# Optimization experiments

Measured on AMD Instinct MI355X. Metric: run time of the kernel, lower is better.

Reference implementation:

```python
import jax, jax.numpy as jnp
import numpy as np

H = 1024       # hidden_size
I = 1024       # intermediate_size
E = 16         # num_experts
K = 4          # experts_per_token
LIMIT = 7.0    # swiglu_limit
ALPHA = 1.702  # swiglu alpha
EPS = 1e-5     # rmsnorm eps


def setup_inputs() -> dict:
    key = jax.random.key(0)
    ks = jax.random.split(key, 8)
    x = jax.random.normal(ks[0], (2, 512, H), dtype=jnp.float32)
    norm_scale = jnp.ones((H,), dtype=jnp.float32)
    wg = jax.random.normal(ks[1], (H, E), dtype=jnp.float32) * 0.02
    bg = jax.random.normal(ks[2], (E,), dtype=jnp.float32) * 0.02
    w1 = jax.random.normal(ks[3], (E, H, 2 * I), dtype=jnp.float32) * 0.02
    b1 = jax.random.normal(ks[4], (E, 2 * I), dtype=jnp.float32) * 0.02
    w2 = jax.random.normal(ks[5], (E, I, H), dtype=jnp.float32) * 0.02
    b2 = jax.random.normal(ks[6], (E, H), dtype=jnp.float32) * 0.02
    return {"x": x, "norm_scale": norm_scale, "wg": wg, "bg": bg,
            "w1": w1, "b1": b1, "w2": w2, "b2": b2}


def reference(x, norm_scale, wg, bg, w1, b1, w2, b2):
    shape = x.shape
    xf = x.reshape(-1, shape[-1])                                   # [T, H]
    # RMSNorm (float32 math)
    xn = xf * jax.lax.rsqrt(jnp.mean(xf * xf, axis=-1, keepdims=True) + EPS) * norm_scale
    # router logits + top-k with softmax over selected logits
    logits = xn @ wg + bg                                           # [T, E]
    vals, idx = jax.lax.top_k(logits, K)                            # [T, K]
    gates = jax.nn.softmax(vals, axis=-1)                           # [T, K]
    # dense [T, E] gate matrix (exactly equivalent to gather/scatter grouped GEMM)
    gate_full = jnp.einsum('tke,tk->te', jax.nn.one_hot(idx, E, dtype=gates.dtype), gates)
    # expert FFN 1 + fused swiglu (interleaved gate/linear pairs)
    h = jnp.einsum('th,ehd->etd', xn, w1) + b1[:, None, :]          # [E, T, 2I]
    a = jnp.minimum(h[..., ::2], LIMIT)                             # gate branch
    b = jnp.clip(h[..., 1::2], -LIMIT, LIMIT)                       # linear branch
    s = a * jax.nn.sigmoid(ALPHA * a) * (b + 1.0)                   # [E, T, I]
    # expert FFN 2; gamma (gate) scales the full epilogue incl. bias
    y = jnp.einsum('eti,eih->eth', s, w2) + b2[:, None, :]          # [E, T, H]
    t = jnp.einsum('eth,te->th', y, gate_full)                      # scatter-combine
    return x + t.reshape(shape)
```

## Files before the change

### kernel.cpp

```cpp
#include <hip/hip_runtime.h>

#define NH 1024
#define NI2 2048
#define NI 1024
#define NE 16
#define NT 1024

static constexpr float LIMITF = 7.0f;
static constexpr float ALPHAF = 1.702f;
static constexpr float EPSF = 1e-5f;

typedef short bf16x8 __attribute__((ext_vector_type(8)));
typedef float f32x16 __attribute__((ext_vector_type(16)));

__device__ __forceinline__ unsigned short f2bf(float f) {
  unsigned int u = __builtin_bit_cast(unsigned int, f);
  u = (u + 0x7FFFu + ((u >> 16) & 1u)) >> 16;
  return (unsigned short)u;
}

typedef __attribute__((address_space(1))) const unsigned int as1_uint;
typedef __attribute__((address_space(3))) unsigned int as3_uint;
__device__ __forceinline__ void gload16(const void* g, void* l) {
  __builtin_amdgcn_global_load_lds((as1_uint*)g, (as3_uint*)l, 16, 0, 0);
}

__global__ __launch_bounds__(256) void k_init(const float* __restrict__ x,
                                              float* __restrict__ out) {
  int i = blockIdx.x * 256 + threadIdx.x;
  reinterpret_cast<float4*>(out)[i] = reinterpret_cast<const float4*>(x)[i];
}

__global__ __launch_bounds__(256) void k_norm_router(
    const float* __restrict__ x, const float* __restrict__ nsc,
    const float* __restrict__ wg, const float* __restrict__ bg,
    unsigned short* __restrict__ xn, int* __restrict__ topk_idx,
    float* __restrict__ topk_gate, int* __restrict__ counts) {
  int t = blockIdx.x;
  int tid = threadIdx.x;
  int wave = tid >> 6, lane = tid & 63;

  float4 v = reinterpret_cast<const float4*>(x + (size_t)t * NH)[tid];
  float ss = v.x * v.x + v.y * v.y + v.z * v.z + v.w * v.w;
  for (int off = 32; off; off >>= 1) ss += __shfl_xor(ss, off);

  __shared__ float red[4];
  __shared__ float redl[4][16];
  __shared__ float logits_s[16];
  if (lane == 0) red[wave] = ss;
  __syncthreads();
  float tot = red[0] + red[1] + red[2] + red[3];
  float r = rsqrtf(tot * (1.0f / NH) + EPSF);

  float4 sc = reinterpret_cast<const float4*>(nsc)[tid];
  float xv[4];
  xv[0] = v.x * r * sc.x;
  xv[1] = v.y * r * sc.y;
  xv[2] = v.z * r * sc.z;
  xv[3] = v.w * r * sc.w;

  ushort4 o;
  o.x = f2bf(xv[0]); o.y = f2bf(xv[1]); o.z = f2bf(xv[2]); o.w = f2bf(xv[3]);
  reinterpret_cast<ushort4*>(xn + (size_t)t * NH)[tid] = o;

  float acc[16];
#pragma unroll
  for (int e = 0; e < 16; e++) acc[e] = 0.f;
  int hbase = tid * 4;
#pragma unroll
  for (int i = 0; i < 4; i++) {
    const float4* wr = reinterpret_cast<const float4*>(wg + (size_t)(hbase + i) * NE);
#pragma unroll
    for (int j = 0; j < 4; j++) {
      float4 w = wr[j];
      acc[j * 4 + 0] += xv[i] * w.x;
      acc[j * 4 + 1] += xv[i] * w.y;
      acc[j * 4 + 2] += xv[i] * w.z;
      acc[j * 4 + 3] += xv[i] * w.w;
    }
  }
#pragma unroll
  for (int e = 0; e < 16; e++)
    for (int off = 32; off; off >>= 1) acc[e] += __shfl_xor(acc[e], off);
  if (lane == 0) {
#pragma unroll
    for (int e = 0; e < 16; e++) redl[wave][e] = acc[e];
  }
  __syncthreads();
  if (tid < 16)
    logits_s[tid] = redl[0][tid] + redl[1][tid] + redl[2][tid] + redl[3][tid] + bg[tid];
  __syncthreads();

  if (tid == 0) {
    float vals[16];
#pragma unroll
    for (int e = 0; e < 16; e++) vals[e] = logits_s[e];
    int sel[4]; float sv[4];
    unsigned used = 0;
    for (int k = 0; k < 4; k++) {
      float best = -1e30f; int bi = 0;
      for (int e = 0; e < 16; e++) {
        if (!((used >> e) & 1u) && vals[e] > best) { best = vals[e]; bi = e; }
      }
      used |= 1u << bi; sel[k] = bi; sv[k] = best;
    }
    float g[4], ssum = 0.f;
    for (int k = 0; k < 4; k++) { g[k] = __expf(sv[k] - sv[0]); ssum += g[k]; }
    for (int k = 0; k < 4; k++) {
      topk_idx[t * 4 + k] = sel[k];
      topk_gate[t * 4 + k] = g[k] / ssum;
      atomicAdd(&counts[sel[k]], 1);
    }
  }
}

__global__ void k_scan(const int* __restrict__ counts, int* __restrict__ offsets,
                       int* __restrict__ cursor) {
  if (blockIdx.x == 0 && threadIdx.x == 0) {
    int o = 0;
    for (int e = 0; e < NE; e++) {
      offsets[e] = o; cursor[e] = o;
      o += (counts[e] + 31) & ~31;
    }
  }
}

__global__ __launch_bounds__(256) void k_fill(const int* __restrict__ topk_idx,
                                              const float* __restrict__ topk_gate,
                                              int* __restrict__ cursor,
                                              int* __restrict__ rows_tok,
                                              float* __restrict__ rows_gate) {
  int idx = blockIdx.x * 256 + threadIdx.x;
  if (idx >= NT * 4) return;
  int e = topk_idx[idx];
  int slot = atomicAdd(&cursor[e], 1);
  rows_tok[slot] = idx >> 2;
  rows_gate[slot] = topk_gate[idx];
}

__global__ __launch_bounds__(256) void k_gather(
    const unsigned short* __restrict__ xn, const int* __restrict__ counts,
    const int* __restrict__ offsets, const int* __restrict__ rows_tok,
    unsigned short* __restrict__ xg) {
  int e = blockIdx.y;
  int g = blockIdx.x;
  int cnt = counts[e];
  if (g * 32 >= cnt) return;
  int tid = threadIdx.x;
  int r = tid & 31, kq = tid >> 5;
  int rowbase = offsets[e];
  int tok = rows_tok[rowbase + min(g * 32 + r, cnt - 1)];
  const uint4* src = reinterpret_cast<const uint4*>(xn + (size_t)tok * NH);
  uint4* dst = reinterpret_cast<uint4*>(
      xg + ((size_t)(rowbase >> 5) + g) * (128 * 32 * 8));
#pragma unroll
  for (int i = 0; i < 16; i++) {
    int ko = i * 8 + kq;
    dst[ko * 32 + r] = src[ko];
  }
}

template <int ROWSTRIDE>
__device__ __forceinline__ void stage_panel_async(
    const float* __restrict__ wsrc, unsigned short* __restrict__ panel,
    float* __restrict__ fbuf, int tid) {
  int colq = tid & 7;
  int rquot = tid >> 3;
  int col = tid & 31;
  int oct = tid >> 5;
  for (int r = 0; r < 8; r++) {
#pragma unroll
    for (int i = 0; i < 4; i++) {
      int row = r * 128 + i * 32 + rquot;
      gload16(wsrc + (size_t)row * ROWSTRIDE + colq * 4,
              (char*)fbuf + tid * 16 + i * 4096);
    }
    __syncthreads();
#pragma unroll
    for (int oo = 0; oo < 2; oo++) {
      int o = oct + oo * 8;
      float f[8];
#pragma unroll
      for (int j = 0; j < 8; j++) f[j] = fbuf[(o * 8 + j) * 32 + col];
      unsigned pk[4];
#pragma unroll
      for (int j = 0; j < 4; j++)
        pk[j] = (unsigned)f2bf(f[2 * j]) | ((unsigned)f2bf(f[2 * j + 1]) << 16);
      *reinterpret_cast<uint4*>(&panel[(size_t)((r * 16 + o) * 32 + col) * 8]) =
          *reinterpret_cast<const uint4*>(pk);
    }
    __syncthreads();
  }
}

__global__ __launch_bounds__(256) void k_ffn1(
    const unsigned short* __restrict__ xg, const float* __restrict__ w1,
    const float* __restrict__ b1, const int* __restrict__ counts,
    const int* __restrict__ offsets, unsigned short* __restrict__ s_tiled) {
  int b = blockIdx.x;
  int j = b >> 3;
  int e = (b & 7) + ((j >> 6) << 3);
  int n0 = (j & 63) * 32;
  int cnt = counts[e];
  if (cnt == 0) return;
  int rowbase = offsets[e];
  int tid = threadIdx.x;

  __shared__ __align__(16) unsigned short lds_b[128 * 32 * 8];
  __shared__ __align__(16) float lds_f[128 * 32];

  stage_panel_async<NI2>(w1 + (size_t)e * (NH * NI2) + n0, lds_b, lds_f, tid);

  int lane = tid & 63;
  int wave = tid >> 6;
  int lrow = lane & 31;
  int khalf = lane >> 5;

  float bias = b1[(size_t)e * NI2 + n0 + lrow];
  int parity = lrow & 1;

  for (int m0 = 0; m0 < cnt; m0 += 256) {
    int tb0 = m0 + wave * 32;
    int tb1 = m0 + 128 + wave * 32;
    const unsigned short* a0p =
        xg + ((size_t)((rowbase + tb0) >> 5) * 128 + khalf) * 256 + lrow * 8;

    f32x16 acc0 = {0.f,0.f,0.f,0.f,0.f,0.f,0.f,0.f,0.f,0.f,0.f,0.f,0.f,0.f,0.f,0.f};
    f32x16 acc1 = {0.f,0.f,0.f,0.f,0.f,0.f,0.f,0.f,0.f,0.f,0.f,0.f,0.f,0.f,0.f,0.f};
    bool dual = (m0 + 128) < cnt;

    if (dual) {
      const unsigned short* a1p =
          xg + ((size_t)((rowbase + tb1) >> 5) * 128 + khalf) * 256 + lrow * 8;
#pragma unroll 4
      for (int k2 = 0; k2 < 64; k2++) {
        bf16x8 av0 = *reinterpret_cast<const bf16x8*>(a0p + k2 * 512);
        bf16x8 av1 = *reinterpret_cast<const bf16x8*>(a1p + k2 * 512);
        bf16x8 bv = *reinterpret_cast<const bf16x8*>(
            &lds_b[(size_t)((k2 * 2 + khalf) * 32 + lrow) * 8]);
        acc0 = __builtin_amdgcn_mfma_f32_32x32x16_bf16(av0, bv, acc0, 0, 0, 0);
        acc1 = __builtin_amdgcn_mfma_f32_32x32x16_bf16(av1, bv, acc1, 0, 0, 0);
      }
    } else {
#pragma unroll 4
      for (int k2 = 0; k2 < 64; k2++) {
        bf16x8 av0 = *reinterpret_cast<const bf16x8*>(a0p + k2 * 512);
        bf16x8 bv = *reinterpret_cast<const bf16x8*>(
            &lds_b[(size_t)((k2 * 2 + khalf) * 32 + lrow) * 8]);
        acc0 = __builtin_amdgcn_mfma_f32_32x32x16_bf16(av0, bv, acc0, 0, 0, 0);
      }
    }

#pragma unroll
    for (int t2 = 0; t2 < 2; t2++) {
      if (t2 == 1 && !dual) break;
      f32x16 acc = t2 ? acc1 : acc0;
      int tb = t2 ? tb1 : tb0;
#pragma unroll
      for (int reg = 0; reg < 16; reg++) {
        float v = acc[reg] + bias;
        float p = __shfl_xor(v, 1);
        int row = (reg & 3) + 8 * (reg >> 2) + 4 * khalf;
        int m = tb + row;
        if (!parity && m < cnt) {
          float aa = fminf(v, LIMITF);
          float bb = fminf(fmaxf(p, -LIMITF), LIMITF);
          float sig = 1.0f / (1.0f + __expf(-ALPHAF * aa));
          float sval = aa * sig * (bb + 1.0f);
          int c = (n0 + lrow) >> 1;
          size_t grp = (size_t)(rowbase + tb) >> 5;
          s_tiled[(grp * 128 + (c >> 3)) * 256 + row * 8 + (c & 7)] = f2bf(sval);
        }
      }
    }
  }
}

__global__ __launch_bounds__(256) void k_ffn2(
    const unsigned short* __restrict__ s_tiled, const float* __restrict__ w2,
    const float* __restrict__ b2, const int* __restrict__ counts,
    const int* __restrict__ offsets, const int* __restrict__ rows_tok,
    const float* __restrict__ rows_gate, float* __restrict__ out) {
  int b = blockIdx.x;
  int j = b >> 3;
  int e = (b & 7) + ((j >> 5) << 3);
  int n0 = (j & 31) * 32;
  int cnt = counts[e];
  if (cnt == 0) return;
  int rowbase = offsets[e];
  int tid = threadIdx.x;

  __shared__ __align__(16) unsigned short lds_b[128 * 32 * 8];
  __shared__ __align__(16) float lds_f[128 * 32];

  stage_panel_async<NH>(w2 + (size_t)e * (NI * NH) + n0, lds_b, lds_f, tid);

  int lane = tid & 63;
  int wave = tid >> 6;
  int lrow = lane & 31;
  int khalf = lane >> 5;

  float b2v = b2[(size_t)e * NH + n0 + lrow];

  for (int m0 = 0; m0 < cnt; m0 += 256) {
    int tb0 = m0 + wave * 32;
    int tb1 = m0 + 128 + wave * 32;
    const unsigned short* a0p =
        s_tiled + ((size_t)((rowbase + tb0) >> 5) * 128 + khalf) * 256 + lrow * 8;

    f32x16 acc0 = {0.f,0.f,0.f,0.f,0.f,0.f,0.f,0.f,0.f,0.f,0.f,0.f,0.f,0.f,0.f,0.f};
    f32x16 acc1 = {0.f,0.f,0.f,0.f,0.f,0.f,0.f,0.f,0.f,0.f,0.f,0.f,0.f,0.f,0.f,0.f};
    bool dual = (m0 + 128) < cnt;

    if (dual) {
      const unsigned short* a1p =
          s_tiled + ((size_t)((rowbase + tb1) >> 5) * 128 + khalf) * 256 + lrow * 8;
#pragma unroll 4
      for (int k2 = 0; k2 < 64; k2++) {
        bf16x8 av0 = *reinterpret_cast<const bf16x8*>(a0p + k2 * 512);
        bf16x8 av1 = *reinterpret_cast<const bf16x8*>(a1p + k2 * 512);
        bf16x8 bv = *reinterpret_cast<const bf16x8*>(
            &lds_b[(size_t)((k2 * 2 + khalf) * 32 + lrow) * 8]);
        acc0 = __builtin_amdgcn_mfma_f32_32x32x16_bf16(av0, bv, acc0, 0, 0, 0);
        acc1 = __builtin_amdgcn_mfma_f32_32x32x16_bf16(av1, bv, acc1, 0, 0, 0);
      }
    } else {
#pragma unroll 4
      for (int k2 = 0; k2 < 64; k2++) {
        bf16x8 av0 = *reinterpret_cast<const bf16x8*>(a0p + k2 * 512);
        bf16x8 bv = *reinterpret_cast<const bf16x8*>(
            &lds_b[(size_t)((k2 * 2 + khalf) * 32 + lrow) * 8]);
        acc0 = __builtin_amdgcn_mfma_f32_32x32x16_bf16(av0, bv, acc0, 0, 0, 0);
      }
    }

#pragma unroll
    for (int t2 = 0; t2 < 2; t2++) {
      if (t2 == 1 && !dual) break;
      f32x16 acc = t2 ? acc1 : acc0;
      int tb = t2 ? tb1 : tb0;
#pragma unroll
      for (int reg = 0; reg < 16; reg++) {
        int row = (reg & 3) + 8 * (reg >> 2) + 4 * khalf;
        int m = tb + row;
        if (m < cnt) {
          int rr = rowbase + m;
          int tok = rows_tok[rr];
          float g = rows_gate[rr];
          atomicAdd(&out[(size_t)tok * NH + n0 + lrow], g * (acc[reg] + b2v));
        }
      }
    }
  }
}

extern "C" void kernel_launch(void* const* d_in, const int* in_sizes, int n_in,
                              void* d_out, int out_size, void* d_ws, size_t ws_size,
                              hipStream_t stream) {
  const float* x   = (const float*)d_in[0];
  const float* nsc = (const float*)d_in[1];
  const float* wg  = (const float*)d_in[2];
  const float* bg  = (const float*)d_in[3];
  const float* w1  = (const float*)d_in[4];
  const float* b1  = (const float*)d_in[5];
  const float* w2  = (const float*)d_in[6];
  const float* b2  = (const float*)d_in[7];
  float* out = (float*)d_out;
  char* ws = (char*)d_ws;

  int*   counts    = (int*)(ws + 0);
  int*   offsets   = (int*)(ws + 64);
  int*   cursor    = (int*)(ws + 128);
  int*   topk_idx  = (int*)(ws + 1024);
  float* topk_gate = (float*)(ws + 17408);
  int*   rows_tok  = (int*)(ws + 33792);
  float* rows_gate = (float*)(ws + 54272);
  unsigned short* xn      = (unsigned short*)(ws + 131072);
  unsigned short* xg      = (unsigned short*)(ws + 2228224);
  unsigned short* s_tiled = (unsigned short*)(ws + 12 * 1024 * 1024);

  hipMemsetAsync(ws, 0, 256, stream);
  k_init<<<NT * NH / 1024, 256, 0, stream>>>(x, out);
  k_norm_router<<<NT, 256, 0, stream>>>(x, nsc, wg, bg, xn, topk_idx, topk_gate,
                                        counts);
  k_scan<<<1, 64, 0, stream>>>(counts, offsets, cursor);
  k_fill<<<16, 256, 0, stream>>>(topk_idx, topk_gate, cursor, rows_tok, rows_gate);
  k_gather<<<dim3(128, NE), 256, 0, stream>>>(xn, counts, offsets, rows_tok, xg);
  k_ffn1<<<1024, 256, 0, stream>>>(xg, w1, b1, counts, offsets, s_tiled);
  k_ffn2<<<512, 256, 0, stream>>>(s_tiled, w2, b2, counts, offsets,
                                  rows_tok, rows_gate, out);
}
```

Measured before the change: 430.0 us.

## Use 512-thread blocks with one M-tile per wave and register-prefetched A operands

Both expert GEMM kernels now launch 8 waves per block instead of 4. Each wave handles a single 32-row tile rather than two, and the weight-panel staging is spread across 512 threads. The A-operand loads from global memory go through an 8-deep register prefetch ring, so MFMAs overlap with in-flight loads, aiming to hide global-load latency and raise occupancy. Risks: `__launch_bounds__(512,4)` may squeeze registers and cause spills, the prefetch reads past the end of the K range, and the LDS footprint may cap real occupancy anyway.

```diff
diff --git a/kernel.cpp b/kernel.cpp
--- a/kernel.cpp
+++ b/kernel.cpp
@@ -167,33 +167,29 @@
   int colq = tid & 7;
   int rquot = tid >> 3;
   int col = tid & 31;
-  int oct = tid >> 5;
+  int o = tid >> 5;
   for (int r = 0; r < 8; r++) {
 #pragma unroll
-    for (int i = 0; i < 4; i++) {
-      int row = r * 128 + i * 32 + rquot;
+    for (int i = 0; i < 2; i++) {
+      int row = r * 128 + i * 64 + rquot;
       gload16(wsrc + (size_t)row * ROWSTRIDE + colq * 4,
-              (char*)fbuf + tid * 16 + i * 4096);
+              (char*)fbuf + tid * 16 + i * 8192);
     }
     __syncthreads();
-#pragma unroll
-    for (int oo = 0; oo < 2; oo++) {
-      int o = oct + oo * 8;
-      float f[8];
-#pragma unroll
-      for (int j = 0; j < 8; j++) f[j] = fbuf[(o * 8 + j) * 32 + col];
-      unsigned pk[4];
-#pragma unroll
-      for (int j = 0; j < 4; j++)
-        pk[j] = (unsigned)f2bf(f[2 * j]) | ((unsigned)f2bf(f[2 * j + 1]) << 16);
-      *reinterpret_cast<uint4*>(&panel[(size_t)((r * 16 + o) * 32 + col) * 8]) =
-          *reinterpret_cast<const uint4*>(pk);
-    }
+    float f[8];
+#pragma unroll
+    for (int jj = 0; jj < 8; jj++) f[jj] = fbuf[(o * 8 + jj) * 32 + col];
+    unsigned pk[4];
+#pragma unroll
+    for (int jj = 0; jj < 4; jj++)
+      pk[jj] = (unsigned)f2bf(f[2 * jj]) | ((unsigned)f2bf(f[2 * jj + 1]) << 16);
+    *reinterpret_cast<uint4*>(&panel[(size_t)((r * 16 + o) * 32 + col) * 8]) =
+        *reinterpret_cast<const uint4*>(pk);
     __syncthreads();
   }
 }
 
-__global__ __launch_bounds__(256) void k_ffn1(
+__global__ __launch_bounds__(512, 4) void k_ffn1(
     const unsigned short* __restrict__ xg, const float* __restrict__ w1,
     const float* __restrict__ b1, const int* __restrict__ counts,
     const int* __restrict__ offsets, unsigned short* __restrict__ s_tiled) {
@@ -220,63 +216,47 @@
   int parity = lrow & 1;
 
   for (int m0 = 0; m0 < cnt; m0 += 256) {
-    int tb0 = m0 + wave * 32;
-    int tb1 = m0 + 128 + wave * 32;
-    const unsigned short* a0p =
-        xg + ((size_t)((rowbase + tb0) >> 5) * 128 + khalf) * 256 + lrow * 8;
-
-    f32x16 acc0 = {0.f,0.f,0.f,0.f,0.f,0.f,0.f,0.f,0.f,0.f,0.f,0.f,0.f,0.f,0.f,0.f};
-    f32x16 acc1 = {0.f,0.f,0.f,0.f,0.f,0.f,0.f,0.f,0.f,0.f,0.f,0.f,0.f,0.f,0.f,0.f};
-    bool dual = (m0 + 128) < cnt;
-
-    if (dual) {
-      const unsigned short* a1p =
-          xg + ((size_t)((rowbase + tb1) >> 5) * 128 + khalf) * 256 + lrow * 8;
-#pragma unroll 4
-      for (int k2 = 0; k2 < 64; k2++) {
-        bf16x8 av0 = *reinterpret_cast<const bf16x8*>(a0p + k2 * 512);
-        bf16x8 av1 = *reinterpret_cast<const bf16x8*>(a1p + k2 * 512);
+    int tb = m0 + wave * 32;
+    const unsigned short* ap =
+        xg + ((size_t)((rowbase + tb) >> 5) * 128 + khalf) * 256 + lrow * 8;
+
+    f32x16 acc = {0.f,0.f,0.f,0.f,0.f,0.f,0.f,0.f,0.f,0.f,0.f,0.f,0.f,0.f,0.f,0.f};
+    bf16x8 pre[8];
+#pragma unroll
+    for (int u = 0; u < 8; u++)
+      pre[u] = *reinterpret_cast<const bf16x8*>(ap + u * 512);
+
+    for (int k2 = 0; k2 < 64; k2 += 8) {
+#pragma unroll
+      for (int u = 0; u < 8; u++) {
+        bf16x8 av = pre[u];
+        pre[u] = *reinterpret_cast<const bf16x8*>(ap + (k2 + 8 + u) * 512);
         bf16x8 bv = *reinterpret_cast<const bf16x8*>(
-            &lds_b[(size_t)((k2 * 2 + khalf) * 32 + lrow) * 8]);
-        acc0 = __builtin_amdgcn_mfma_f32_32x32x16_bf16(av0, bv, acc0, 0, 0, 0);
-        acc1 = __builtin_amdgcn_mfma_f32_32x32x16_bf16(av1, bv, acc1, 0, 0, 0);
-      }
-    } else {
-#pragma unroll 4
-      for (int k2 = 0; k2 < 64; k2++) {
-        bf16x8 av0 = *reinterpret_cast<const bf16x8*>(a0p + k2 * 512);
-        bf16x8 bv = *reinterpret_cast<const bf16x8*>(
-            &lds_b[(size_t)((k2 * 2 + khalf) * 32 + lrow) * 8]);
-        acc0 = __builtin_amdgcn_mfma_f32_32x32x16_bf16(av0, bv, acc0, 0, 0, 0);
-      }
-    }
-
-#pragma unroll
-    for (int t2 = 0; t2 < 2; t2++) {
-      if (t2 == 1 && !dual) break;
-      f32x16 acc = t2 ? acc1 : acc0;
-      int tb = t2 ? tb1 : tb0;
-#pragma unroll
-      for (int reg = 0; reg < 16; reg++) {
-        float v = acc[reg] + bias;
-        float p = __shfl_xor(v, 1);
-        int row = (reg & 3) + 8 * (reg >> 2) + 4 * khalf;
-        int m = tb + row;
-        if (!parity && m < cnt) {
-          float aa = fminf(v, LIMITF);
-          float bb = fminf(fmaxf(p, -LIMITF), LIMITF);
-          float sig = 1.0f / (1.0f + __expf(-ALPHAF * aa));
-          float sval = aa * sig * (bb + 1.0f);
-          int c = (n0 + lrow) >> 1;
-          size_t grp = (size_t)(rowbase + tb) >> 5;
-          s_tiled[(grp * 128 + (c >> 3)) * 256 + row * 8 + (c & 7)] = f2bf(sval);
-        }
-      }
-    }
-  }
-}
-
-__global__ __launch_bounds__(256) void k_ffn2(
+            &lds_b[(size_t)(((k2 + u) * 2 + khalf) * 32 + lrow) * 8]);
+        acc = __builtin_amdgcn_mfma_f32_32x32x16_bf16(av, bv, acc, 0, 0, 0);
+      }
+    }
+
+#pragma unroll
+    for (int reg = 0; reg < 16; reg++) {
+      float v = acc[reg] + bias;
+      float p = __shfl_xor(v, 1);
+      int row = (reg & 3) + 8 * (reg >> 2) + 4 * khalf;
+      int m = tb + row;
+      if (!parity && m < cnt) {
+        float aa = fminf(v, LIMITF);
+        float bb = fminf(fmaxf(p, -LIMITF), LIMITF);
+        float sig = 1.0f / (1.0f + __expf(-ALPHAF * aa));
+        float sval = aa * sig * (bb + 1.0f);
+        int c = (n0 + lrow) >> 1;
+        size_t grp = (size_t)(rowbase + tb) >> 5;
+        s_tiled[(grp * 128 + (c >> 3)) * 256 + row * 8 + (c & 7)] = f2bf(sval);
+      }
+    }
+  }
+}
+
+__global__ __launch_bounds__(512, 4) void k_ffn2(
     const unsigned short* __restrict__ s_tiled, const float* __restrict__ w2,
     const float* __restrict__ b2, const int* __restrict__ counts,
     const int* __restrict__ offsets, const int* __restrict__ rows_tok,
@@ -303,52 +283,36 @@
   float b2v = b2[(size_t)e * NH + n0 + lrow];
 
   for (int m0 = 0; m0 < cnt; m0 += 256) {
-    int tb0 = m0 + wave * 32;
-    int tb1 = m0 + 128 + wave * 32;
-    const unsigned short* a0p =
-        s_tiled + ((size_t)((rowbase + tb0) >> 5) * 128 + khalf) * 256 + lrow * 8;
-
-    f32x16 acc0 = {0.f,0.f,0.f,0.f,0.f,0.f,0.f,0.f,0.f,0.f,0.f,0.f,0.f,0.f,0.f,0.f};
-    f32x16 acc1 = {0.f,0.f,0.f,0.f,0.f,0.f,0.f,0.f,0.f,0.f,0.f,0.f,0.f,0.f,0.f,0.f};
-    bool dual = (m0 + 128) < cnt;
-
-    if (dual) {
-      const unsigned short* a1p =
-          s_tiled + ((size_t)((rowbase + tb1) >> 5) * 128 + khalf) * 256 + lrow * 8;
-#pragma unroll 4
-      for (int k2 = 0; k2 < 64; k2++) {
-        bf16x8 av0 = *reinterpret_cast<const bf16x8*>(a0p + k2 * 512);
-        bf16x8 av1 = *reinterpret_cast<const bf16x8*>(a1p + k2 * 512);
+    int tb = m0 + wave * 32;
+    const unsigned short* ap =
+        s_tiled + ((size_t)((rowbase + tb) >> 5) * 128 + khalf) * 256 + lrow * 8;
+
+    f32x16 acc = {0.f,0.f,0.f,0.f,0.f,0.f,0.f,0.f,0.f,0.f,0.f,0.f,0.f,0.f,0.f,0.f};
+    bf16x8 pre[8];
+#pragma unroll
+    for (int u = 0; u < 8; u++)
+      pre[u] = *reinterpret_cast<const bf16x8*>(ap + u * 512);
+
+    for (int k2 = 0; k2 < 64; k2 += 8) {
+#pragma unroll
+      for (int u = 0; u < 8; u++) {
+        bf16x8 av = pre[u];
+        pre[u] = *reinterpret_cast<const bf16x8*>(ap + (k2 + 8 + u) * 512);
         bf16x8 bv = *reinterpret_cast<const bf16x8*>(
-            &lds_b[(size_t)((k2 * 2 + khalf) * 32 + lrow) * 8]);
-        acc0 = __builtin_amdgcn_mfma_f32_32x32x16_bf16(av0, bv, acc0, 0, 0, 0);
-        acc1 = __builtin_amdgcn_mfma_f32_32x32x16_bf16(av1, bv, acc1, 0, 0, 0);
-      }
-    } else {
-#pragma unroll 4
-      for (int k2 = 0; k2 < 64; k2++) {
-        bf16x8 av0 = *reinterpret_cast<const bf16x8*>(a0p + k2 * 512);
-        bf16x8 bv = *reinterpret_cast<const bf16x8*>(
-            &lds_b[(size_t)((k2 * 2 + khalf) * 32 + lrow) * 8]);
-        acc0 = __builtin_amdgcn_mfma_f32_32x32x16_bf16(av0, bv, acc0, 0, 0, 0);
-      }
-    }
-
-#pragma unroll
-    for (int t2 = 0; t2 < 2; t2++) {
-      if (t2 == 1 && !dual) break;
-      f32x16 acc = t2 ? acc1 : acc0;
-      int tb = t2 ? tb1 : tb0;
-#pragma unroll
-      for (int reg = 0; reg < 16; reg++) {
-        int row = (reg & 3) + 8 * (reg >> 2) + 4 * khalf;
-        int m = tb + row;
-        if (m < cnt) {
-          int rr = rowbase + m;
-          int tok = rows_tok[rr];
-          float g = rows_gate[rr];
-          atomicAdd(&out[(size_t)tok * NH + n0 + lrow], g * (acc[reg] + b2v));
-        }
+            &lds_b[(size_t)(((k2 + u) * 2 + khalf) * 32 + lrow) * 8]);
+        acc = __builtin_amdgcn_mfma_f32_32x32x16_bf16(av, bv, acc, 0, 0, 0);
+      }
+    }
+
+#pragma unroll
+    for (int reg = 0; reg < 16; reg++) {
+      int row = (reg & 3) + 8 * (reg >> 2) + 4 * khalf;
+      int m = tb + row;
+      if (m < cnt) {
+        int rr = rowbase + m;
+        int tok = rows_tok[rr];
+        float g = rows_gate[rr];
+        atomicAdd(&out[(size_t)tok * NH + n0 + lrow], g * (acc[reg] + b2v));
       }
     }
   }
@@ -386,7 +350,7 @@
   k_scan<<<1, 64, 0, stream>>>(counts, offsets, cursor);
   k_fill<<<16, 256, 0, stream>>>(topk_idx, topk_gate, cursor, rows_tok, rows_gate);
   k_gather<<<dim3(128, NE), 256, 0, stream>>>(xn, counts, offsets, rows_tok, xg);
-  k_ffn1<<<1024, 256, 0, stream>>>(xg, w1, b1, counts, offsets, s_tiled);
-  k_ffn2<<<512, 256, 0, stream>>>(s_tiled, w2, b2, counts, offsets,
+  k_ffn1<<<1024, 512, 0, stream>>>(xg, w1, b1, counts, offsets, s_tiled);
+  k_ffn2<<<512, 512, 0, stream>>>(s_tiled, w2, b2, counts, offsets,
                                   rows_tok, rows_gate, out);
 }
```

Measured after the change: 662.7 us. +54.1%, slower.
